# Optimization experiments

Measured on AMD Instinct MI355X. Metric: run time of the kernel, lower is better.

Reference implementation:

```python
import jax, jax.numpy as jnp
import numpy as np

USER_NUM = 100000
ITEM_NUM = 50000
E = 128   # embedding_size
A = 64    # attention_size
M = 8     # memory_size
B = 4096  # batch
NF = 50   # friends per user


def _l2norm(x, axis):
    # torch F.normalize(p=2): x / max(||x||, eps)
    n = jnp.sqrt(jnp.sum(x * x, axis=axis, keepdims=True))
    return x / jnp.maximum(n, 1e-12)


def setup_inputs() -> dict:
    key = jax.random.key(0)
    ks = jax.random.split(key, 9)
    u = lambda k, shape: jax.random.uniform(k, shape, jnp.float32, -0.1, 0.1)
    return {
        "input_u": jax.random.randint(ks[0], (B,), 0, USER_NUM),
        "input_i": jax.random.randint(ks[1], (B,), 0, ITEM_NUM),
        "input_uf": jax.random.randint(ks[2], (B, NF), 0, USER_NUM + 1),
        "uidW": u(ks[3], (USER_NUM + 1, E)),
        "iidW": u(ks[4], (ITEM_NUM, E)),
        "i_bias": jnp.zeros((ITEM_NUM,), jnp.float32),
        "Key": u(ks[5], (E, M)),
        "Mem": jnp.ones((M, E), jnp.float32),
        "WA": u(ks[6], (E, A)),
        "BA": jnp.zeros((A,), jnp.float32),
        "U_omega": u(ks[7], (A, 1)),
    }


def reference(input_u, input_i, input_uf, uidW, iidW, i_bias, Key, Mem, WA, BA, U_omega):
    user_num = uidW.shape[0] - 1  # padding id
    uid = uidW[input_u]                      # [B, E]
    iid = iidW[input_i]                      # [B, E]
    i_b = i_bias[input_i]                    # [B]
    fe = uidW[input_uf]                      # [B, F, E] friend embeddings
    fn = (input_uf != user_num).astype(uid.dtype)  # [B, F] valid-friend mask

    fe = fn[:, :, None] * fe
    uid_n = _l2norm(uid, axis=1)
    fe_n = _l2norm(fe, axis=2)
    cross = uid_n[:, None, :] * fe_n                     # [B, F, E]
    att_key = jnp.einsum('bfe,em->bfm', cross, Key)      # [B, F, M]
    att_mem = jax.nn.softmax(att_key, axis=0)            # softmax over batch (faithful to dim=0)
    att_mem = fn[:, :, None] * att_mem
    f1 = jnp.einsum('bfm,me->bfe', att_mem, Mem)         # [B, F, E]
    f2 = f1 * fe
    h = jax.nn.relu(jnp.einsum('bfe,ea->bfa', f2, WA) + BA)
    j = jnp.exp(jnp.einsum('bfa,ao->bfo', h, U_omega))   # [B, F, 1]
    j = fn[:, :, None] * j
    w = j / (jnp.sum(j, axis=1, keepdims=True) + 1e-8)
    friend = jnp.sum(w * f2, axis=1)                     # [B, E] (dropout p=0 -> identity)
    user = uid + friend
    score = jnp.sum(user * iid, axis=1) + i_b            # [B]
    return score
```

## Files before the change

kernel.cpp:

```cpp
#include <hip/hip_runtime.h>

#define EDIM 128
#define MDIM 8
#define ADIM 64
#define NFR  50
#define NCOL (NFR * MDIM)
#define NPART 64

typedef __attribute__((ext_vector_type(8))) short short8;
typedef __attribute__((ext_vector_type(4))) float f32x4;

__device__ __forceinline__ float waveReduceSum(float v) {
    #pragma unroll
    for (int s = 32; s >= 1; s >>= 1) v += __shfl_xor(v, s, 64);
    return v;
}
__device__ __forceinline__ short f2bf(float x) {
    unsigned u = __float_as_uint(x);
    u += 0x7FFFu + ((u >> 16) & 1u);
    return (short)(u >> 16);
}
__device__ __forceinline__ float bf2f(short s) {
    return __uint_as_float(((unsigned)(unsigned short)s) << 16);
}

__global__ __launch_bounds__(256)
void k0_all(const float* __restrict__ uidW, const float* __restrict__ WA,
            const float* __restrict__ Mem, const float* __restrict__ Key,
            short* __restrict__ ubW, short* __restrict__ WATf,
            short* __restrict__ MemTf, short* __restrict__ KeyTf,
            float* __restrict__ S, int nU, int cvtBlocks)
{
    int blk = blockIdx.x;
    if (blk < cvtBlocks) {
        int idx = (blk * 256 + threadIdx.x) * 8;
        if (idx < nU) {
            float4 a = *(const float4*)(uidW + idx);
            float4 b = *(const float4*)(uidW + idx + 4);
            short8 v;
            v[0] = f2bf(a.x); v[1] = f2bf(a.y); v[2] = f2bf(a.z); v[3] = f2bf(a.w);
            v[4] = f2bf(b.x); v[5] = f2bf(b.y); v[6] = f2bf(b.z); v[7] = f2bf(b.w);
            *(short8*)(ubW + idx) = v;
        }
        return;
    }
    int t = (blk - cvtBlocks) * 256 + threadIdx.x;
    int lane = t & 63, c = lane & 15, g = (lane >> 4) & 3;
    short8 v = {0, 0, 0, 0, 0, 0, 0, 0};
    if (t < 1024) {
        int frag = t >> 6, Ma = frag >> 2, Kt = frag & 3;
        int a = Ma * 16 + c;
        #pragma unroll
        for (int j = 0; j < 8; ++j) {
            int e = Kt * 32 + g * 8 + j;
            v[j] = f2bf(WA[(size_t)e * ADIM + a]);
        }
        *(short8*)(WATf + (size_t)t * 8) = v;
    } else if (t < 1536) {
        int i = t - 1024, Mt = i >> 6;
        int e = Mt * 16 + c;
        #pragma unroll
        for (int j = 0; j < 8; ++j) {
            int k = g * 8 + j;
            v[j] = (k < MDIM) ? f2bf(Mem[(size_t)k * EDIM + e]) : (short)0;
        }
        *(short8*)(MemTf + (size_t)i * 8) = v;
    } else if (t < 1792) {
        int i = t - 1536, Kt = i >> 6;
        #pragma unroll
        for (int j = 0; j < 8; ++j) {
            int e = Kt * 32 + g * 8 + j;
            v[j] = (c < MDIM) ? f2bf(Key[(size_t)e * MDIM + c]) : (short)0;
        }
        *(short8*)(KeyTf + (size_t)i * 8) = v;
    } else if (t < 1792 + NCOL) {
        S[t - 1792] = 0.f;
    }
}

__global__ __launch_bounds__(256, 8)
void k1_attkey(const int* __restrict__ input_u, const int* __restrict__ input_uf,
               const short* __restrict__ ubW, const short* __restrict__ KeyTf,
               float* __restrict__ eatt, int user_num)
{
    const int b = blockIdx.x, t = threadIdx.x, w = t >> 6, l = t & 63;
    const int c = l & 15, g = l >> 4;
    __shared__ float uidn[EDIM];
    __shared__ float redW[4];
    __shared__ int ufL[64];

    if (t < 64) ufL[t] = (t < NFR) ? input_uf[(size_t)b * NFR + t] : user_num;
    const int u = input_u[b];
    float x = (t < EDIM) ? bf2f(ubW[(size_t)u * EDIM + t]) : 0.f;
    float ss = waveReduceSum(x * x);
    if (l == 0) redW[w] = ss;
    __syncthreads();
    float uinv = 1.0f / fmaxf(sqrtf(redW[0] + redW[1] + redW[2] + redW[3]), 1e-12f);
    if (t < EDIM) uidn[t] = x * uinv;
    __syncthreads();

    const int f = w * 16 + c;
    const int fid = ufL[f];
    const float fn = (f < NFR && fid != user_num) ? 1.0f : 0.0f;
    const short* fp = ubW + (size_t)fid * EDIM;

    short8 feb[4];
    #pragma unroll
    for (int Kt = 0; Kt < 4; ++Kt)
        feb[Kt] = *(const short8*)(fp + Kt * 32 + g * 8);

    float fef[4][8];
    float fss = 0.f;
    #pragma unroll
    for (int Kt = 0; Kt < 4; ++Kt)
        #pragma unroll
        for (int j = 0; j < 8; ++j) {
            float q = bf2f(feb[Kt][j]);
            fef[Kt][j] = q;
            fss += q * q;
        }
    fss += __shfl_xor(fss, 16, 64);
    fss += __shfl_xor(fss, 32, 64);
    const float inv2 = fn / fmaxf(sqrtf(fss), 1e-12f);

    f32x4 acc = {0.f, 0.f, 0.f, 0.f};
    #pragma unroll
    for (int Kt = 0; Kt < 4; ++Kt) {
        const float* un = &uidn[Kt * 32 + g * 8];
        short8 bf;
        #pragma unroll
        for (int j = 0; j < 8; ++j)
            bf[j] = f2bf(un[j] * fef[Kt][j] * inv2);
        short8 af = *(const short8*)(KeyTf + (size_t)(Kt * 64 + l) * 8);
        acc = __builtin_amdgcn_mfma_f32_16x16x32_bf16(af, bf, acc, 0, 0, 0);
    }
    if (f < NFR && g < 2) {
        float4 st = {__expf(acc[0]), __expf(acc[1]), __expf(acc[2]), __expf(acc[3])};
        *(float4*)&eatt[(size_t)b * NCOL + f * MDIM + g * 4] = st;
    }
}

__global__ __launch_bounds__(256)
void k2a_sum(const float* __restrict__ eatt, float* __restrict__ S, int B)
{
    const int blk = blockIdx.x, t = threadIdx.x, w = t >> 6, l = t & 63;
    __shared__ float colS[4][NCOL];
    const int rowsPerBlk = B / NPART;
    const int rowsPerWave = rowsPerBlk >> 2;
    const int r0 = blk * rowsPerBlk + w * rowsPerWave;

    float4 a1 = {0.f, 0.f, 0.f, 0.f}, a2 = {0.f, 0.f, 0.f, 0.f};
    for (int it = 0; it < rowsPerWave; ++it) {
        const float* row = eatt + (size_t)(r0 + it) * NCOL;
        float4 v1 = *(const float4*)(row + 4 * l);
        a1.x += v1.x; a1.y += v1.y; a1.z += v1.z; a1.w += v1.w;
        if (l < 36) {
            float4 v2 = *(const float4*)(row + 256 + 4 * l);
            a2.x += v2.x; a2.y += v2.y; a2.z += v2.z; a2.w += v2.w;
        }
    }
    *(float4*)&colS[w][4 * l] = a1;
    if (l < 36) *(float4*)&colS[w][256 + 4 * l] = a2;
    __syncthreads();
    for (int i = t; i < NCOL; i += 256)
        atomicAdd(&S[i], colS[0][i] + colS[1][i] + colS[2][i] + colS[3][i]);
}

__global__ __launch_bounds__(256, 6)
void k3_final(const int* __restrict__ input_u, const int* __restrict__ input_i,
              const int* __restrict__ input_uf, const float* __restrict__ uidW,
              const float* __restrict__ iidW, const float* __restrict__ i_bias,
              const short* __restrict__ WATf, const short* __restrict__ MemTf,
              const float* __restrict__ BA, const float* __restrict__ U_omega,
              const float* __restrict__ eatt, const float* __restrict__ S,
              const short* __restrict__ ubW, float* __restrict__ out,
              int user_num)
{
    const int b = blockIdx.x, t = threadIdx.x, w = t >> 6, l = t & 63;
    const int c = l & 15, g = l >> 4;
    __shared__ short f2s[4][4 * 64 * 8];
    __shared__ float uidL[EDIM], iidL[EDIM];
    __shared__ float baL[ADIM], uoL[ADIM];
    __shared__ int ufL[64];
    __shared__ float sjW[4], syW[4];

    if (t < 64) ufL[t] = (t < NFR) ? input_uf[(size_t)b * NFR + t] : user_num;
    const int u = input_u[b];
    const int ii = input_i[b];
    if (t < EDIM) {
        uidL[t] = uidW[(size_t)u * EDIM + t];
        iidL[t] = iidW[(size_t)ii * EDIM + t];
    }
    if (t < ADIM) { baL[t] = BA[t]; uoL[t] = U_omega[t]; }
    __syncthreads();

    const int f = w * 16 + c;
    const int fid = ufL[f];
    const float fn = (f < NFR && fid != user_num) ? 1.0f : 0.0f;
    const short* fp3 = ubW + (size_t)fid * EDIM;

    short8 amf = {0, 0, 0, 0, 0, 0, 0, 0};
    if (g == 0 && fn > 0.f) {
        const float* ea = eatt + (size_t)b * NCOL + f * 8;
        float4 e0 = *(const float4*)ea;
        float4 e1 = *(const float4*)(ea + 4);
        float4 s0 = *(const float4*)&S[f * 8];
        float4 s1 = *(const float4*)&S[f * 8 + 4];
        amf[0] = f2bf(e0.x * __builtin_amdgcn_rcpf(s0.x));
        amf[1] = f2bf(e0.y * __builtin_amdgcn_rcpf(s0.y));
        amf[2] = f2bf(e0.z * __builtin_amdgcn_rcpf(s0.z));
        amf[3] = f2bf(e0.w * __builtin_amdgcn_rcpf(s0.w));
        amf[4] = f2bf(e1.x * __builtin_amdgcn_rcpf(s1.x));
        amf[5] = f2bf(e1.y * __builtin_amdgcn_rcpf(s1.y));
        amf[6] = f2bf(e1.z * __builtin_amdgcn_rcpf(s1.z));
        amf[7] = f2bf(e1.w * __builtin_amdgcn_rcpf(s1.w));
    }

    f32x4 C1[8];
    #pragma unroll
    for (int Mt = 0; Mt < 8; ++Mt) {
        short8 af = *(const short8*)(MemTf + (size_t)(Mt * 64 + l) * 8);
        f32x4 z = {0.f, 0.f, 0.f, 0.f};
        C1[Mt] = __builtin_amdgcn_mfma_f32_16x16x32_bf16(af, amf, z, 0, 0, 0);
    }

    #pragma unroll
    for (int Mt = 0; Mt < 8; ++Mt) {
        uint2 fv = *(const uint2*)(fp3 + Mt * 16 + g * 4);
        float q0 = C1[Mt][0] * bf2f((short)(fv.x & 0xFFFF));
        float q1 = C1[Mt][1] * bf2f((short)(fv.x >> 16));
        float q2 = C1[Mt][2] * bf2f((short)(fv.y & 0xFFFF));
        float q3 = C1[Mt][3] * bf2f((short)(fv.y >> 16));
        unsigned d0 = ((unsigned)(unsigned short)f2bf(q0)) |
                      (((unsigned)(unsigned short)f2bf(q1)) << 16);
        unsigned d1 = ((unsigned)(unsigned short)f2bf(q2)) |
                      (((unsigned)(unsigned short)f2bf(q3)) << 16);
        int lane2 = ((Mt & 1) * 2 + (g >> 1)) * 16 + c;
        int off = ((Mt >> 1) * 64 + lane2) * 8 + (g & 1) * 4;
        uint2 dd = {d0, d1};
        *(uint2*)&f2s[w][off] = dd;
    }

    f32x4 C2[4], C3 = {0.f, 0.f, 0.f, 0.f};
    #pragma unroll
    for (int Ma = 0; Ma < 4; ++Ma) C2[Ma] = (f32x4){0.f, 0.f, 0.f, 0.f};
    #pragma unroll
    for (int Kt = 0; Kt < 4; ++Kt) {
        short8 bf = *(const short8*)&f2s[w][(Kt * 64 + l) * 8];
        #pragma unroll
        for (int Ma = 0; Ma < 4; ++Ma) {
            short8 af = *(const short8*)(WATf + (size_t)((Ma * 4 + Kt) * 64 + l) * 8);
            C2[Ma] = __builtin_amdgcn_mfma_f32_16x16x32_bf16(af, bf, C2[Ma], 0, 0, 0);
        }
        short8 itf = {0, 0, 0, 0, 0, 0, 0, 0};
        if (c == 0) {
            float4 i0 = *(const float4*)&iidL[Kt * 32 + g * 8];
            float4 i1 = *(const float4*)&iidL[Kt * 32 + g * 8 + 4];
            itf[0] = f2bf(i0.x); itf[1] = f2bf(i0.y);
            itf[2] = f2bf(i0.z); itf[3] = f2bf(i0.w);
            itf[4] = f2bf(i1.x); itf[5] = f2bf(i1.y);
            itf[6] = f2bf(i1.z); itf[7] = f2bf(i1.w);
        }
        C3 = __builtin_amdgcn_mfma_f32_16x16x32_bf16(itf, bf, C3, 0, 0, 0);
    }

    float psum = 0.f;
    #pragma unroll
    for (int Ma = 0; Ma < 4; ++Ma) {
        float4 ba4 = *(const float4*)&baL[Ma * 16 + g * 4];
        float4 uo4 = *(const float4*)&uoL[Ma * 16 + g * 4];
        psum += fmaxf(C2[Ma][0] + ba4.x, 0.f) * uo4.x;
        psum += fmaxf(C2[Ma][1] + ba4.y, 0.f) * uo4.y;
        psum += fmaxf(C2[Ma][2] + ba4.z, 0.f) * uo4.z;
        psum += fmaxf(C2[Ma][3] + ba4.w, 0.f) * uo4.w;
    }
    psum += __shfl_xor(psum, 16, 64);
    psum += __shfl_xor(psum, 32, 64);
    const float jv = (fn > 0.f) ? __expf(psum) : 0.f;
    const float jy = jv * C3[0];
    float sj = waveReduceSum((g == 0) ? jv : 0.f);
    float sy = waveReduceSum(jy);
    if (l == 0) { sjW[w] = sj; syW[w] = sy; }
    __syncthreads();

    if (w == 0) {
        float s = uidL[l] * iidL[l] + uidL[l + 64] * iidL[l + 64];
        s = waveReduceSum(s);
        if (l == 0) {
            float Sj = sjW[0] + sjW[1] + sjW[2] + sjW[3] + 1e-8f;
            float Sy = syW[0] + syW[1] + syW[2] + syW[3];
            out[b] = s + Sy / Sj + i_bias[ii];
        }
    }
}

extern "C" void kernel_launch(void* const* d_in, const int* in_sizes, int n_in,
                              void* d_out, int out_size, void* d_ws, size_t ws_size,
                              hipStream_t stream)
{
    const int*   input_u  = (const int*)d_in[0];
    const int*   input_i  = (const int*)d_in[1];
    const int*   input_uf = (const int*)d_in[2];
    const float* uidW     = (const float*)d_in[3];
    const float* iidW     = (const float*)d_in[4];
    const float* i_bias   = (const float*)d_in[5];
    const float* Key      = (const float*)d_in[6];
    const float* Mem      = (const float*)d_in[7];
    const float* WA       = (const float*)d_in[8];
    const float* BA       = (const float*)d_in[9];
    const float* U_om     = (const float*)d_in[10];

    const int B = in_sizes[0];
    const int nU = in_sizes[3];
    const int user_num = nU / EDIM - 1;

    float* eatt = (float*)d_ws;
    float* S    = eatt + (size_t)B * NCOL;
    short* WATf  = (short*)(S + NCOL);
    short* MemTf = WATf + 16 * 64 * 8;
    short* KeyTf = MemTf + 8 * 64 * 8;
    short* ubW   = KeyTf + 4 * 64 * 8;

    const int cvtBlocks = (nU / 8 + 255) / 256;
    k0_all<<<cvtBlocks + 9, 256, 0, stream>>>(uidW, WA, Mem, Key,
                                              ubW, WATf, MemTf, KeyTf, S,
                                              nU, cvtBlocks);
    k1_attkey<<<B, 256, 0, stream>>>(input_u, input_uf, ubW, KeyTf, eatt, user_num);
    k2a_sum<<<NPART, 256, 0, stream>>>(eatt, S, B);
    k3_final<<<B, 256, 0, stream>>>(input_u, input_i, input_uf, uidW, iidW, i_bias,
                                    WATf, MemTf, BA, U_om, eatt, S, ubW,
                                    (float*)d_out, user_num);
}
```

Before: 173.8 us.

## Fuse column-sum into attkey kernel with two rows per block, prefetch friend rows

The separate column-sum kernel is removed. The attention-key kernel now handles two batch rows per block and atomically adds their exp values straight into the global column sums. The final kernel hoists the friend-embedding loads ahead of the first MFMA, and it reads the user row directly in wave 0 instead of staging it in shared memory. This saves one launch and one full re-read of eatt, but adds many contended atomics (about 2048 blocks hitting 400 addresses) and a nondeterministic summation order.

```diff
diff --git a/kernel.cpp b/kernel.cpp
--- a/kernel.cpp
+++ b/kernel.cpp
@@ -5,7 +5,6 @@
 #define ADIM 64
 #define NFR  50
 #define NCOL (NFR * MDIM)
-#define NPART 64
 
 typedef __attribute__((ext_vector_type(8))) short short8;
 typedef __attribute__((ext_vector_type(4))) float f32x4;
@@ -78,92 +77,87 @@
     }
 }
 
-__global__ __launch_bounds__(256, 8)
+__global__ __launch_bounds__(256, 4)
 void k1_attkey(const int* __restrict__ input_u, const int* __restrict__ input_uf,
                const short* __restrict__ ubW, const short* __restrict__ KeyTf,
-               float* __restrict__ eatt, int user_num)
+               float* __restrict__ eatt, float* __restrict__ S, int user_num)
 {
-    const int b = blockIdx.x, t = threadIdx.x, w = t >> 6, l = t & 63;
+    const int blk = blockIdx.x;
+    const int b0 = blk * 2, b1 = b0 + 1;
+    const int t = threadIdx.x, w = t >> 6, l = t & 63;
     const int c = l & 15, g = l >> 4;
-    __shared__ float uidn[EDIM];
+    __shared__ float uidn0[EDIM], uidn1[EDIM];
     __shared__ float redW[4];
-    __shared__ int ufL[64];
-
-    if (t < 64) ufL[t] = (t < NFR) ? input_uf[(size_t)b * NFR + t] : user_num;
-    const int u = input_u[b];
-    float x = (t < EDIM) ? bf2f(ubW[(size_t)u * EDIM + t]) : 0.f;
+    __shared__ int ufL0[64], ufL1[64];
+
+    if (t < 64) ufL0[t] = (t < NFR) ? input_uf[(size_t)b0 * NFR + t] : user_num;
+    else if (t < 128) {
+        int q = t - 64;
+        ufL1[q] = (q < NFR) ? input_uf[(size_t)b1 * NFR + q] : user_num;
+    }
+    const int ub = input_u[(t < 128) ? b0 : b1];
+    const int eI = t & 127;
+    float x = bf2f(ubW[(size_t)ub * EDIM + eI]);
     float ss = waveReduceSum(x * x);
     if (l == 0) redW[w] = ss;
     __syncthreads();
-    float uinv = 1.0f / fmaxf(sqrtf(redW[0] + redW[1] + redW[2] + redW[3]), 1e-12f);
-    if (t < EDIM) uidn[t] = x * uinv;
+    float nrm = (t < 128) ? (redW[0] + redW[1]) : (redW[2] + redW[3]);
+    float uin = 1.0f / fmaxf(sqrtf(nrm), 1e-12f);
+    if (t < 128) uidn0[eI] = x * uin; else uidn1[eI] = x * uin;
     __syncthreads();
 
     const int f = w * 16 + c;
-    const int fid = ufL[f];
-    const float fn = (f < NFR && fid != user_num) ? 1.0f : 0.0f;
-    const short* fp = ubW + (size_t)fid * EDIM;
-
-    short8 feb[4];
+    const int fid0 = ufL0[f], fid1 = ufL1[f];
+    const float fn0 = (f < NFR && fid0 != user_num) ? 1.0f : 0.0f;
+    const float fn1 = (f < NFR && fid1 != user_num) ? 1.0f : 0.0f;
+    const short* fp0 = ubW + (size_t)fid0 * EDIM;
+    const short* fp1 = ubW + (size_t)fid1 * EDIM;
+
+    short8 fe0[4], fe1[4];
+    #pragma unroll
+    for (int Kt = 0; Kt < 4; ++Kt) {
+        fe0[Kt] = *(const short8*)(fp0 + Kt * 32 + g * 8);
+        fe1[Kt] = *(const short8*)(fp1 + Kt * 32 + g * 8);
+    }
+    float fss0 = 0.f, fss1 = 0.f;
     #pragma unroll
     for (int Kt = 0; Kt < 4; ++Kt)
-        feb[Kt] = *(const short8*)(fp + Kt * 32 + g * 8);
-
-    float fef[4][8];
-    float fss = 0.f;
-    #pragma unroll
-    for (int Kt = 0; Kt < 4; ++Kt)
-        #pragma unroll
-        for (int j = 0; j < 8; ++j) {
-            float q = bf2f(feb[Kt][j]);
-            fef[Kt][j] = q;
-            fss += q * q;
-        }
-    fss += __shfl_xor(fss, 16, 64);
-    fss += __shfl_xor(fss, 32, 64);
-    const float inv2 = fn / fmaxf(sqrtf(fss), 1e-12f);
-
-    f32x4 acc = {0.f, 0.f, 0.f, 0.f};
+        #pragma unroll
+        for (int j = 0; j < 8; ++j) {
+            float q0 = bf2f(fe0[Kt][j]); fss0 += q0 * q0;
+            float q1 = bf2f(fe1[Kt][j]); fss1 += q1 * q1;
+        }
+    fss0 += __shfl_xor(fss0, 16, 64); fss0 += __shfl_xor(fss0, 32, 64);
+    fss1 += __shfl_xor(fss1, 16, 64); fss1 += __shfl_xor(fss1, 32, 64);
+    const float inv0 = fn0 / fmaxf(sqrtf(fss0), 1e-12f);
+    const float inv1 = fn1 / fmaxf(sqrtf(fss1), 1e-12f);
+
+    f32x4 acc0 = {0.f, 0.f, 0.f, 0.f}, acc1 = {0.f, 0.f, 0.f, 0.f};
     #pragma unroll
     for (int Kt = 0; Kt < 4; ++Kt) {
-        const float* un = &uidn[Kt * 32 + g * 8];
-        short8 bf;
-        #pragma unroll
-        for (int j = 0; j < 8; ++j)
-            bf[j] = f2bf(un[j] * fef[Kt][j] * inv2);
+        const float* un0 = &uidn0[Kt * 32 + g * 8];
+        const float* un1 = &uidn1[Kt * 32 + g * 8];
+        short8 bf0, bf1;
+        #pragma unroll
+        for (int j = 0; j < 8; ++j) {
+            bf0[j] = f2bf(un0[j] * bf2f(fe0[Kt][j]) * inv0);
+            bf1[j] = f2bf(un1[j] * bf2f(fe1[Kt][j]) * inv1);
+        }
         short8 af = *(const short8*)(KeyTf + (size_t)(Kt * 64 + l) * 8);
-        acc = __builtin_amdgcn_mfma_f32_16x16x32_bf16(af, bf, acc, 0, 0, 0);
+        acc0 = __builtin_amdgcn_mfma_f32_16x16x32_bf16(af, bf0, acc0, 0, 0, 0);
+        acc1 = __builtin_amdgcn_mfma_f32_16x16x32_bf16(af, bf1, acc1, 0, 0, 0);
     }
     if (f < NFR && g < 2) {
-        float4 st = {__expf(acc[0]), __expf(acc[1]), __expf(acc[2]), __expf(acc[3])};
-        *(float4*)&eatt[(size_t)b * NCOL + f * MDIM + g * 4] = st;
-    }
-}
-
-__global__ __launch_bounds__(256)
-void k2a_sum(const float* __restrict__ eatt, float* __restrict__ S, int B)
-{
-    const int blk = blockIdx.x, t = threadIdx.x, w = t >> 6, l = t & 63;
-    __shared__ float colS[4][NCOL];
-    const int rowsPerBlk = B / NPART;
-    const int rowsPerWave = rowsPerBlk >> 2;
-    const int r0 = blk * rowsPerBlk + w * rowsPerWave;
-
-    float4 a1 = {0.f, 0.f, 0.f, 0.f}, a2 = {0.f, 0.f, 0.f, 0.f};
-    for (int it = 0; it < rowsPerWave; ++it) {
-        const float* row = eatt + (size_t)(r0 + it) * NCOL;
-        float4 v1 = *(const float4*)(row + 4 * l);
-        a1.x += v1.x; a1.y += v1.y; a1.z += v1.z; a1.w += v1.w;
-        if (l < 36) {
-            float4 v2 = *(const float4*)(row + 256 + 4 * l);
-            a2.x += v2.x; a2.y += v2.y; a2.z += v2.z; a2.w += v2.w;
-        }
-    }
-    *(float4*)&colS[w][4 * l] = a1;
-    if (l < 36) *(float4*)&colS[w][256 + 4 * l] = a2;
-    __syncthreads();
-    for (int i = t; i < NCOL; i += 256)
-        atomicAdd(&S[i], colS[0][i] + colS[1][i] + colS[2][i] + colS[3][i]);
+        float4 e0 = {__expf(acc0[0]), __expf(acc0[1]), __expf(acc0[2]), __expf(acc0[3])};
+        float4 e1 = {__expf(acc1[0]), __expf(acc1[1]), __expf(acc1[2]), __expf(acc1[3])};
+        *(float4*)&eatt[(size_t)b0 * NCOL + f * MDIM + g * 4] = e0;
+        *(float4*)&eatt[(size_t)b1 * NCOL + f * MDIM + g * 4] = e1;
+        float* sp = S + f * MDIM + g * 4;
+        atomicAdd(sp + 0, e0.x + e1.x);
+        atomicAdd(sp + 1, e0.y + e1.y);
+        atomicAdd(sp + 2, e0.z + e1.z);
+        atomicAdd(sp + 3, e0.w + e1.w);
+    }
 }
 
 __global__ __launch_bounds__(256, 6)
@@ -179,18 +173,14 @@
     const int b = blockIdx.x, t = threadIdx.x, w = t >> 6, l = t & 63;
     const int c = l & 15, g = l >> 4;
     __shared__ short f2s[4][4 * 64 * 8];
-    __shared__ float uidL[EDIM], iidL[EDIM];
+    __shared__ float iidL[EDIM];
     __shared__ float baL[ADIM], uoL[ADIM];
     __shared__ int ufL[64];
     __shared__ float sjW[4], syW[4];
 
     if (t < 64) ufL[t] = (t < NFR) ? input_uf[(size_t)b * NFR + t] : user_num;
-    const int u = input_u[b];
     const int ii = input_i[b];
-    if (t < EDIM) {
-        uidL[t] = uidW[(size_t)u * EDIM + t];
-        iidL[t] = iidW[(size_t)ii * EDIM + t];
-    }
+    if (t < EDIM) iidL[t] = iidW[(size_t)ii * EDIM + t];
     if (t < ADIM) { baL[t] = BA[t]; uoL[t] = U_omega[t]; }
     __syncthreads();
 
@@ -198,6 +188,11 @@
     const int fid = ufL[f];
     const float fn = (f < NFR && fid != user_num) ? 1.0f : 0.0f;
     const short* fp3 = ubW + (size_t)fid * EDIM;
+
+    uint2 fv[8];
+    #pragma unroll
+    for (int Mt = 0; Mt < 8; ++Mt)
+        fv[Mt] = *(const uint2*)(fp3 + Mt * 16 + g * 4);
 
     short8 amf = {0, 0, 0, 0, 0, 0, 0, 0};
     if (g == 0 && fn > 0.f) {
@@ -226,11 +221,10 @@
 
     #pragma unroll
     for (int Mt = 0; Mt < 8; ++Mt) {
-        uint2 fv = *(const uint2*)(fp3 + Mt * 16 + g * 4);
-        float q0 = C1[Mt][0] * bf2f((short)(fv.x & 0xFFFF));
-        float q1 = C1[Mt][1] * bf2f((short)(fv.x >> 16));
-        float q2 = C1[Mt][2] * bf2f((short)(fv.y & 0xFFFF));
-        float q3 = C1[Mt][3] * bf2f((short)(fv.y >> 16));
+        float q0 = C1[Mt][0] * bf2f((short)(fv[Mt].x & 0xFFFF));
+        float q1 = C1[Mt][1] * bf2f((short)(fv[Mt].x >> 16));
+        float q2 = C1[Mt][2] * bf2f((short)(fv[Mt].y & 0xFFFF));
+        float q3 = C1[Mt][3] * bf2f((short)(fv[Mt].y >> 16));
         unsigned d0 = ((unsigned)(unsigned short)f2bf(q0)) |
                       (((unsigned)(unsigned short)f2bf(q1)) << 16);
         unsigned d1 = ((unsigned)(unsigned short)f2bf(q2)) |
@@ -284,7 +278,9 @@
     __syncthreads();
 
     if (w == 0) {
-        float s = uidL[l] * iidL[l] + uidL[l + 64] * iidL[l + 64];
+        const int u = input_u[b];
+        float s = uidW[(size_t)u * EDIM + l] * iidL[l]
+                + uidW[(size_t)u * EDIM + 64 + l] * iidL[64 + l];
         s = waveReduceSum(s);
         if (l == 0) {
             float Sj = sjW[0] + sjW[1] + sjW[2] + sjW[3] + 1e-8f;
@@ -325,8 +321,8 @@
     k0_all<<<cvtBlocks + 9, 256, 0, stream>>>(uidW, WA, Mem, Key,
                                               ubW, WATf, MemTf, KeyTf, S,
                                               nU, cvtBlocks);
-    k1_attkey<<<B, 256, 0, stream>>>(input_u, input_uf, ubW, KeyTf, eatt, user_num);
-    k2a_sum<<<NPART, 256, 0, stream>>>(eatt, S, B);
+    k1_attkey<<<B / 2, 256, 0, stream>>>(input_u, input_uf, ubW, KeyTf,
+                                         eatt, S, user_num);
     k3_final<<<B, 256, 0, stream>>>(input_u, input_i, input_uf, uidW, iidW, i_bias,
                                     WATf, MemTf, BA, U_om, eatt, S, ubW,
                                     (float*)d_out, user_num);
```

New measurement: 357.6 us. 106% more time.
